# Kernel tuning notes

Measured on AMD Instinct MI355X. Metric: run time of the kernel, lower is better.

Reference implementation:

```python
import jax, jax.numpy as jnp
import numpy as np

B = 262144
D = 26  # lip_dim + pose_dim
OUT = 512


def setup_inputs() -> dict:
    key = jax.random.key(0)
    k1, k2 = jax.random.split(key)
    input = jax.random.normal(k1, (B, D), dtype=jnp.float32)
    weight = jax.random.normal(k2, (OUT, D), dtype=jnp.float32)
    return {"input": input, "weight": weight}


def reference(input, weight):
    # weight: [512, d]; reduced QR -> Q: [512, d]
    w = weight + 1e-8
    Q, _ = jnp.linalg.qr(w)
    # torch: sum(diag_embed(input) @ Q.T, dim=1) == input @ Q.T  -> [B, 512]
    out = jnp.einsum('bd,od->bo', input, Q)
    return out
```

## Files before the change

### kernel.cpp

```cpp
#include <hip/hip_runtime.h>
#include <math.h>

#define QR_M 512
#define QR_N 26
#define OUTC 512
#define LDP 30

using half8_t = __attribute__((ext_vector_type(8))) _Float16;
using f32x4   = __attribute__((ext_vector_type(4))) float;

__global__ __launch_bounds__(512) void qr_kernel(const float* __restrict__ w,
                                                 _Float16* __restrict__ qf) {
  const int tid  = threadIdx.x;
  const int lane = tid & 63;
  const int wid  = tid >> 6;

  __shared__ float As[QR_M][LDP];
  __shared__ float Gs[QR_N][LDP];
  __shared__ float Rt[QR_N][LDP];
  __shared__ float Gp[4][91][4];

  {
    const float2* wp = reinterpret_cast<const float2*>(w + (size_t)tid * QR_N);
    float2 v[13];
#pragma unroll
    for (int i = 0; i < 13; ++i) v[i] = wp[i];
#pragma unroll
    for (int i = 0; i < 13; ++i) {
      As[tid][2 * i]     = v[i].x + 1e-8f;
      As[tid][2 * i + 1] = v[i].y + 1e-8f;
    }
  }
  __syncthreads();

  if (tid < 364) {
    const int chunk = tid / 91;
    const int blk   = tid - chunk * 91;
    int cb = 0, rem = blk;
    while (rem >= 13 - cb) { rem -= 13 - cb; ++cb; }
    const int db = cb + rem;
    const int c0 = 2 * cb, d0 = 2 * db;
    float s00 = 0.f, s01 = 0.f, s10 = 0.f, s11 = 0.f;
    const int r0 = chunk * 128;
    for (int r = r0; r < r0 + 128; ++r) {
      const float2 ac = *reinterpret_cast<const float2*>(&As[r][c0]);
      const float2 ad = *reinterpret_cast<const float2*>(&As[r][d0]);
      s00 += ac.x * ad.x; s01 += ac.x * ad.y;
      s10 += ac.y * ad.x; s11 += ac.y * ad.y;
    }
    Gp[chunk][blk][0] = s00; Gp[chunk][blk][1] = s01;
    Gp[chunk][blk][2] = s10; Gp[chunk][blk][3] = s11;
  }
  __syncthreads();

  if (tid < 364) {
    const int blk = tid >> 2;
    const int v   = tid & 3;
    int cb = 0, rem = blk;
    while (rem >= 13 - cb) { rem -= 13 - cb; ++cb; }
    const int db = cb + rem;
    const float s = Gp[0][blk][v] + Gp[1][blk][v] + Gp[2][blk][v] + Gp[3][blk][v];
    const int c = 2 * cb + (v >> 1);
    const int d = 2 * db + (v & 1);
    Gs[c][d] = s;
    Gs[d][c] = s;
  }
  __syncthreads();

  if (wid == 0) {
    const int c  = lane;
    const int cm = (c < QR_N) ? c : (QR_N - 1);
    float gcol[QR_N], tcol[QR_N], rcol[QR_N];
#pragma unroll
    for (int r = 0; r < QR_N; ++r) gcol[r] = Gs[r][cm];
#pragma unroll
    for (int r = 0; r < QR_N; ++r) tcol[r] = As[r][cm];
#pragma unroll
    for (int r = 0; r < QR_N; ++r) rcol[r] = 0.0f;

#pragma unroll
    for (int j = 0; j < QR_N; ++j) {
      float tg = gcol[j];
#pragma unroll
      for (int r = 0; r < QR_N; ++r) {
        if (r < j) tg -= __shfl(rcol[r], j) * rcol[r];
      }
      const float nsq   = __shfl(tg, j);
      const float alpha = __shfl(tcol[j], j);
      const float norm  = sqrtf(nsq);
      const float beta  = (alpha >= 0.0f) ? -norm : norm;
      const float tau   = (beta - alpha) / beta;
      const float scale = 1.0f / (alpha - beta);
      const float wc    = (tg - beta * tcol[j]) * scale;
      const float tw    = (c > j) ? (tau * wc) : 0.0f;
      tcol[j] -= tw;
      rcol[j]  = (c == j) ? beta : tcol[j];
#pragma unroll
      for (int rr = 0; rr < QR_N; ++rr) {
        if (rr > j) {
          const float vtop = __shfl(tcol[rr], j) * scale;
          tcol[rr] -= tw * vtop;
        }
      }
      if (c >= j && c < QR_N) Rt[c][j] = rcol[j];
    }
  }
  __syncthreads();

  float rinv[QR_N];
#pragma unroll
  for (int cc = 0; cc < QR_N; ++cc) rinv[cc] = 1.0f / Rt[cc][cc];

  float y[QR_N];
#pragma unroll
  for (int cc = 0; cc < QR_N; ++cc) y[cc] = As[tid][cc];
#pragma unroll
  for (int cc = 0; cc < QR_N; ++cc) {
    float s = y[cc];
    int k = 0;
#pragma unroll
    for (; k + 1 < cc; k += 2) {
      const float2 rk = *reinterpret_cast<const float2*>(&Rt[cc][k]);
      s -= y[k] * rk.x + y[k + 1] * rk.y;
    }
    if (k < cc) s -= y[k] * Rt[cc][k];
    y[cc] = s * rinv[cc];
  }

  half8_t h0, h1, h2, h3;
#pragma unroll
  for (int e = 0; e < 8; ++e) h0[e] = (_Float16)y[e];
#pragma unroll
  for (int e = 0; e < 8; ++e) h1[e] = (_Float16)y[8 + e];
#pragma unroll
  for (int e = 0; e < 8; ++e) h2[e] = (_Float16)y[16 + e];
  h3[0] = (_Float16)y[24]; h3[1] = (_Float16)y[25];
#pragma unroll
  for (int e = 2; e < 8; ++e) h3[e] = (_Float16)0.0f;
  half8_t* qrow = reinterpret_cast<half8_t*>(qf + (size_t)tid * 32);
  qrow[0] = h0; qrow[1] = h1; qrow[2] = h2; qrow[3] = h3;
}

__global__ __launch_bounds__(256, 4) void dir_matmul(const float* __restrict__ x,
                                                     const _Float16* __restrict__ qf,
                                                     float* __restrict__ out,
                                                     int nblk32) {
  const int tid   = threadIdx.x;
  const int wid   = tid >> 6;
  const int l     = tid & 63;
  const int rloc  = l & 15;
  const int grp   = l >> 4;
  const int k0    = grp * 8;
  const int rhalf = (wid >> 1) * 16;
  const int chalf = (wid & 1) * 256;
  const int t2b   = (wid & 1) * 16;

  __shared__ float tile[4][16 * 132];
  float* tw = tile[wid];

  half8_t bq[16];
#pragma unroll
  for (int t2 = 0; t2 < 16; ++t2)
    bq[t2] = *reinterpret_cast<const half8_t*>(
        qf + (size_t)((t2b + t2) * 16 + rloc) * 32 + k0);

  for (int rb = blockIdx.x; rb < nblk32; rb += gridDim.x) {
    const int row = rb * 32 + rhalf + rloc;
    half8_t av;
    const float* xp = x + (size_t)row * QR_N + k0;
    if (grp < 3) {
#pragma unroll
      for (int e = 0; e < 4; ++e) {
        float2 v = *reinterpret_cast<const float2*>(xp + 2 * e);
        av[2 * e]     = (_Float16)v.x;
        av[2 * e + 1] = (_Float16)v.y;
      }
    } else {
      float2 v = *reinterpret_cast<const float2*>(xp);
      av[0] = (_Float16)v.x; av[1] = (_Float16)v.y;
#pragma unroll
      for (int e = 2; e < 8; ++e) av[e] = (_Float16)0.0f;
    }

#pragma unroll
    for (int cc = 0; cc < 2; ++cc) {
#pragma unroll
      for (int tt = 0; tt < 8; ++tt) {
        f32x4 acc = {0.0f, 0.0f, 0.0f, 0.0f};
        acc = __builtin_amdgcn_mfma_f32_16x16x32_f16(av, bq[cc * 8 + tt], acc, 0, 0, 0);
#pragma unroll
        for (int j = 0; j < 4; ++j)
          tw[(grp * 4 + j) * 132 + tt * 16 + rloc] = acc[j];
      }
#pragma unroll
      for (int it = 0; it < 8; ++it) {
        const int r  = it * 2 + (l >> 5);
        const int cg = l & 31;
        f32x4 v = *reinterpret_cast<const f32x4*>(&tw[r * 132 + 4 * cg]);
        *reinterpret_cast<f32x4*>(
            out + (size_t)(rb * 32 + rhalf + r) * OUTC + chalf + cc * 128 + 4 * cg) = v;
      }
    }
  }
}

extern "C" void kernel_launch(void* const* d_in, const int* in_sizes, int n_in,
                              void* d_out, int out_size, void* d_ws, size_t ws_size,
                              hipStream_t stream) {
  const float* input  = (const float*)d_in[0];
  const float* weight = (const float*)d_in[1];
  float* out = (float*)d_out;
  _Float16* qf = (_Float16*)d_ws;

  const int B = in_sizes[0] / QR_N;
  const int nblk32 = B / 32;

  qr_kernel<<<1, 512, 0, stream>>>(weight, qf);
  dir_matmul<<<2048, 256, 0, stream>>>(input, qf, out, nblk32);
}
```

Baseline: 139.0 us.

## Split Gram matrix computation across multiple blocks before single-block QR solve

The Gram matrix reduction moves out of the single-block QR kernel into a new 16-block kernel that writes partial sums to workspace, and the QR kernel then adds them up and keeps weight rows in registers instead of shared memory. The intent is to shorten the serial single-block prologue ahead of the big matmul. It costs one extra kernel launch and a global round trip. Separately, block-wide barriers are added around the per-wave staging tile in the matmul, even though each wave uses its own tile, so this adds synchronisation overhead.

```diff
diff --git a/kernel.cpp b/kernel.cpp
--- a/kernel.cpp
+++ b/kernel.cpp
@@ -9,17 +9,42 @@
 using half8_t = __attribute__((ext_vector_type(8))) _Float16;
 using f32x4   = __attribute__((ext_vector_type(4))) float;
 
-__global__ __launch_bounds__(512) void qr_kernel(const float* __restrict__ w,
-                                                 _Float16* __restrict__ qf) {
+__global__ __launch_bounds__(448) void gram_part(const float* __restrict__ w,
+                                                 float* __restrict__ gp) {
+  __shared__ float Ab[32][27];
+  const int tid = threadIdx.x;
+  const int b   = blockIdx.x;
+  if (tid < 416) {
+    const int r  = tid / 13;
+    const int c2 = tid - r * 13;
+    const float2 v = *reinterpret_cast<const float2*>(
+        w + (size_t)(b * 32 + r) * QR_N + 2 * c2);
+    Ab[r][2 * c2]     = v.x + 1e-8f;
+    Ab[r][2 * c2 + 1] = v.y + 1e-8f;
+  }
+  __syncthreads();
+  if (tid < 351) {
+    int cb = 0, rem = tid;
+    while (rem >= QR_N - cb) { rem -= QR_N - cb; ++cb; }
+    const int d = cb + rem;
+    float s = 0.0f;
+#pragma unroll
+    for (int r = 0; r < 32; ++r) s += Ab[r][cb] * Ab[r][d];
+    gp[b * 351 + tid] = s;
+  }
+}
+
+__global__ __launch_bounds__(512) void qr_solve(const float* __restrict__ w,
+                                                const float* __restrict__ gp,
+                                                _Float16* __restrict__ qf) {
   const int tid  = threadIdx.x;
   const int lane = tid & 63;
   const int wid  = tid >> 6;
 
-  __shared__ float As[QR_M][LDP];
   __shared__ float Gs[QR_N][LDP];
   __shared__ float Rt[QR_N][LDP];
-  __shared__ float Gp[4][91][4];
-
+
+  float y[QR_N];
   {
     const float2* wp = reinterpret_cast<const float2*>(w + (size_t)tid * QR_N);
     float2 v[13];
@@ -27,43 +52,20 @@
     for (int i = 0; i < 13; ++i) v[i] = wp[i];
 #pragma unroll
     for (int i = 0; i < 13; ++i) {
-      As[tid][2 * i]     = v[i].x + 1e-8f;
-      As[tid][2 * i + 1] = v[i].y + 1e-8f;
-    }
-  }
-  __syncthreads();
-
-  if (tid < 364) {
-    const int chunk = tid / 91;
-    const int blk   = tid - chunk * 91;
-    int cb = 0, rem = blk;
-    while (rem >= 13 - cb) { rem -= 13 - cb; ++cb; }
-    const int db = cb + rem;
-    const int c0 = 2 * cb, d0 = 2 * db;
-    float s00 = 0.f, s01 = 0.f, s10 = 0.f, s11 = 0.f;
-    const int r0 = chunk * 128;
-    for (int r = r0; r < r0 + 128; ++r) {
-      const float2 ac = *reinterpret_cast<const float2*>(&As[r][c0]);
-      const float2 ad = *reinterpret_cast<const float2*>(&As[r][d0]);
-      s00 += ac.x * ad.x; s01 += ac.x * ad.y;
-      s10 += ac.y * ad.x; s11 += ac.y * ad.y;
-    }
-    Gp[chunk][blk][0] = s00; Gp[chunk][blk][1] = s01;
-    Gp[chunk][blk][2] = s10; Gp[chunk][blk][3] = s11;
-  }
-  __syncthreads();
-
-  if (tid < 364) {
-    const int blk = tid >> 2;
-    const int v   = tid & 3;
-    int cb = 0, rem = blk;
-    while (rem >= 13 - cb) { rem -= 13 - cb; ++cb; }
-    const int db = cb + rem;
-    const float s = Gp[0][blk][v] + Gp[1][blk][v] + Gp[2][blk][v] + Gp[3][blk][v];
-    const int c = 2 * cb + (v >> 1);
-    const int d = 2 * db + (v & 1);
-    Gs[c][d] = s;
-    Gs[d][c] = s;
+      y[2 * i]     = v[i].x + 1e-8f;
+      y[2 * i + 1] = v[i].y + 1e-8f;
+    }
+  }
+
+  if (tid < 351) {
+    float acc = 0.0f;
+#pragma unroll
+    for (int b = 0; b < 16; ++b) acc += gp[b * 351 + tid];
+    int cb = 0, rem = tid;
+    while (rem >= QR_N - cb) { rem -= QR_N - cb; ++cb; }
+    const int d = cb + rem;
+    Gs[cb][d] = acc;
+    Gs[d][cb] = acc;
   }
   __syncthreads();
 
@@ -74,7 +76,7 @@
 #pragma unroll
     for (int r = 0; r < QR_N; ++r) gcol[r] = Gs[r][cm];
 #pragma unroll
-    for (int r = 0; r < QR_N; ++r) tcol[r] = As[r][cm];
+    for (int r = 0; r < QR_N; ++r) tcol[r] = w[r * QR_N + cm] + 1e-8f;
 #pragma unroll
     for (int r = 0; r < QR_N; ++r) rcol[r] = 0.0f;
 
@@ -111,9 +113,6 @@
 #pragma unroll
   for (int cc = 0; cc < QR_N; ++cc) rinv[cc] = 1.0f / Rt[cc][cc];
 
-  float y[QR_N];
-#pragma unroll
-  for (int cc = 0; cc < QR_N; ++cc) y[cc] = As[tid][cc];
 #pragma unroll
   for (int cc = 0; cc < QR_N; ++cc) {
     float s = y[cc];
@@ -192,6 +191,7 @@
         for (int j = 0; j < 4; ++j)
           tw[(grp * 4 + j) * 132 + tt * 16 + rloc] = acc[j];
       }
+      __syncthreads();
 #pragma unroll
       for (int it = 0; it < 8; ++it) {
         const int r  = it * 2 + (l >> 5);
@@ -200,6 +200,7 @@
         *reinterpret_cast<f32x4*>(
             out + (size_t)(rb * 32 + rhalf + r) * OUTC + chalf + cc * 128 + 4 * cg) = v;
       }
+      __syncthreads();
     }
   }
 }
@@ -210,11 +211,14 @@
   const float* input  = (const float*)d_in[0];
   const float* weight = (const float*)d_in[1];
   float* out = (float*)d_out;
-  _Float16* qf = (_Float16*)d_ws;
+
+  float*    gp = (float*)d_ws;
+  _Float16* qf = (_Float16*)((char*)d_ws + 24576);
 
   const int B = in_sizes[0] / QR_N;
   const int nblk32 = B / 32;
 
-  qr_kernel<<<1, 512, 0, stream>>>(weight, qf);
+  gram_part<<<16, 448, 0, stream>>>(weight, gp);
+  qr_solve<<<1, 512, 0, stream>>>(weight, gp, qf);
   dir_matmul<<<2048, 256, 0, stream>>>(input, qf, out, nblk32);
 }
```

New measurement: 138.5 us. Within noise of the previous version (-0.4%).
